# Performance work log

Hardware: AMD Instinct MI355X
Metric: run time of the kernel (lower is better)

## Reference

```python
import jax, jax.numpy as jnp
import numpy as np

B, T, C = 32, 2048, 1024  # batch, seq_len (<= block_size), n_embd
HEAD_SIZE = 128


def setup_inputs() -> dict:
    key = jax.random.key(0)
    kx, kk, kq, kv = jax.random.split(key, 4)
    std = 0.02  # CustomLinear init: normal(0, 0.02)
    return {
        "x": jax.random.normal(kx, (B, T, C), dtype=jnp.float32),
        "Wk": jax.random.normal(kk, (HEAD_SIZE, C), dtype=jnp.float32) * std,
        "Wq": jax.random.normal(kq, (HEAD_SIZE, C), dtype=jnp.float32) * std,
        "Wv": jax.random.normal(kv, (HEAD_SIZE, C), dtype=jnp.float32) * std,
    }


def reference(x, Wk, Wq, Wv):
    # x: [B, T, C]; W*: [head_size, C] (torch Linear layout, no bias)
    Bb, Tt, Cc = x.shape
    k = jnp.einsum("btc,hc->bth", x, Wk)
    q = jnp.einsum("btc,hc->bth", x, Wq)
    v = jnp.einsum("btc,hc->bth", x, Wv)
    # NOTE: original scales by C**-0.5 (n_embd), not head_size**-0.5
    wei = jnp.einsum("bth,bsh->bts", q, k) * (Cc ** -0.5)
    causal = jnp.tril(jnp.ones((Tt, Tt), dtype=bool))  # tril[:T,:T]
    wei = jnp.where(causal, wei, -jnp.inf)
    wei = jax.nn.softmax(wei, axis=-1)
    return jnp.einsum("bts,bsh->bth", wei, v)  # [B, T, head_size]
```

## Files before the change

### kernel.cpp

```cpp
#include <hip/hip_runtime.h>
#include <hip/hip_bf16.h>

typedef __bf16 bf8_t __attribute__((ext_vector_type(8)));
typedef __bf16 bf4_t __attribute__((ext_vector_type(4)));
typedef float f4_t __attribute__((ext_vector_type(4)));

#define B_ 32
#define T_ 2048
#define C_ 1024
#define H_ 128

__global__ __launch_bounds__(256) void wconv_kernel(
    const float* __restrict__ Wk, const float* __restrict__ Wq, const float* __restrict__ Wv,
    __bf16* __restrict__ Wb)
{
    const int e = (blockIdx.x * 256 + threadIdx.x) * 8;
    const int arr = e >> 17;
    const int off = e & 131071;
    const float* W = (arr == 0) ? Wk : (arr == 1) ? Wq : Wv;
    float4 f0 = *(const float4*)(W + off);
    float4 f1 = *(const float4*)(W + off + 4);
    bf8_t o;
    o[0] = (__bf16)f0.x; o[1] = (__bf16)f0.y; o[2] = (__bf16)f0.z; o[3] = (__bf16)f0.w;
    o[4] = (__bf16)f1.x; o[5] = (__bf16)f1.y; o[6] = (__bf16)f1.z; o[7] = (__bf16)f1.w;
    *(bf8_t*)(Wb + e) = o;
}

__global__ __launch_bounds__(256, 3) void proj_kernel(
    const float* __restrict__ x, const __bf16* __restrict__ Wb,
    __bf16* __restrict__ Kb, __bf16* __restrict__ Qb, __bf16* __restrict__ VtG)
{
    __shared__ __bf16 Xs[64][40];
    __shared__ __bf16 Ws[384][40];

    const int m0   = blockIdx.x * 64;
    const int tid  = threadIdx.x;
    const int lane = tid & 63;
    const int wn   = tid >> 6;
    const int lr   = lane & 15;
    const int quad = lane >> 4;

    f4_t acc[4][6];
    #pragma unroll
    for (int mi = 0; mi < 4; mi++)
        for (int ni = 0; ni < 6; ni++) acc[mi][ni] = f4_t{0.f, 0.f, 0.f, 0.f};

    float4 xr[2];
    bf8_t  wr[6];
    #pragma unroll
    for (int i = 0; i < 2; i++) {
        const int u = tid + i * 256;
        xr[i] = *(const float4*)(x + (size_t)(m0 + (u >> 3)) * C_ + ((u & 7) << 2));
    }
    #pragma unroll
    for (int i = 0; i < 6; i++) {
        const int u = tid + i * 256;
        wr[i] = *(const bf8_t*)(Wb + (size_t)(u >> 2) * C_ + ((u & 3) << 3));
    }

    for (int kkI = 0; kkI < 32; kkI++) {
        __syncthreads();
        #pragma unroll
        for (int i = 0; i < 2; i++) {
            const int u = tid + i * 256;
            float4 f = xr[i];
            *(bf4_t*)&Xs[u >> 3][(u & 7) << 2] =
                bf4_t{(__bf16)f.x, (__bf16)f.y, (__bf16)f.z, (__bf16)f.w};
        }
        #pragma unroll
        for (int i = 0; i < 6; i++) {
            const int u = tid + i * 256;
            *(bf8_t*)&Ws[u >> 2][(u & 3) << 3] = wr[i];
        }
        __syncthreads();
        if (kkI < 31) {
            const int kk = (kkI + 1) * 32;
            #pragma unroll
            for (int i = 0; i < 2; i++) {
                const int u = tid + i * 256;
                xr[i] = *(const float4*)(x + (size_t)(m0 + (u >> 3)) * C_ + kk + ((u & 7) << 2));
            }
            #pragma unroll
            for (int i = 0; i < 6; i++) {
                const int u = tid + i * 256;
                wr[i] = *(const bf8_t*)(Wb + (size_t)(u >> 2) * C_ + kk + ((u & 3) << 3));
            }
        }
        bf8_t xa[4];
        #pragma unroll
        for (int mi = 0; mi < 4; mi++) xa[mi] = *(const bf8_t*)&Xs[mi * 16 + lr][quad * 8];
        #pragma unroll
        for (int ni = 0; ni < 6; ni++) {
            bf8_t wb = *(const bf8_t*)&Ws[ni * 64 + wn * 16 + lr][quad * 8];
            if (ni < 4) {
                #pragma unroll
                for (int mi = 0; mi < 4; mi++)
                    acc[mi][ni] = __builtin_amdgcn_mfma_f32_16x16x32_bf16(xa[mi], wb, acc[mi][ni], 0, 0, 0);
            } else {
                #pragma unroll
                for (int mi = 0; mi < 4; mi++)
                    acc[mi][ni] = __builtin_amdgcn_mfma_f32_16x16x32_bf16(wb, xa[mi], acc[mi][ni], 0, 0, 0);
            }
        }
    }

    const int bb = m0 >> 11;
    const int t0 = m0 & (T_ - 1);
    #pragma unroll
    for (int ni = 0; ni < 4; ni++) {
        __bf16* Out = (ni < 2) ? Kb : Qb;
        const int col = (ni & 1) * 64 + wn * 16 + lr;
        #pragma unroll
        for (int mi = 0; mi < 4; mi++)
            for (int r = 0; r < 4; r++) {
                const int row = m0 + mi * 16 + quad * 4 + r;
                Out[(size_t)row * H_ + col] = (__bf16)acc[mi][ni][r];
            }
    }
    #pragma unroll
    for (int ni = 4; ni < 6; ni++)
        for (int mi = 0; mi < 4; mi++) {
            const int tok = t0 + mi * 16 + lr;
            #pragma unroll
            for (int r = 0; r < 4; r++) {
                const int h = (ni - 4) * 64 + wn * 16 + quad * 4 + r;
                VtG[(size_t)bb * H_ * T_ + (size_t)h * T_ + tok] = (__bf16)acc[mi][ni][r];
            }
        }
}

__global__ __launch_bounds__(512, 4) void flash_kernel(
    const __bf16* __restrict__ Qb, const __bf16* __restrict__ Kb,
    const __bf16* __restrict__ VtG, float* __restrict__ Out)
{
    __shared__ __bf16 Ks[64][136];
    __shared__ __bf16 Vt[128][72];
    __shared__ __bf16 Ps[128][72];

    const int qt = (blockIdx.y < 16) ? (15 - blockIdx.x) : blockIdx.x;
    const int b  = blockIdx.y;
    const size_t kqbase = (size_t)b * T_ * H_;
    const size_t vbase  = (size_t)b * H_ * T_;

    const int tid  = threadIdx.x;
    const int lane = tid & 63;
    const int w    = tid >> 6;
    const int lr   = lane & 15;
    const int quad = lane >> 4;

    bf8_t qf[4];
    {
        const __bf16* qp = Qb + kqbase + (size_t)(qt * 128 + w * 16 + lr) * H_ + quad * 8;
        #pragma unroll
        for (int ks = 0; ks < 4; ks++) qf[ks] = *(const bf8_t*)(qp + ks * 32);
    }

    f4_t o[8];
    #pragma unroll
    for (int n = 0; n < 8; n++) o[n] = f4_t{0.f, 0.f, 0.f, 0.f};
    float ls[4] = {0.f, 0.f, 0.f, 0.f};

    const float sc = 0.03125f * 1.4426950408889634f;
    const int jmax = 2 * qt + 1;

    const int kRow0 = tid >> 4,          kC0 = (tid & 15) << 3;
    const int kRow1 = (tid + 512) >> 4,  kC1 = ((tid + 512) & 15) << 3;
    const int vH0 = tid >> 3,            vS0 = (tid & 7) << 3;
    const int vH1 = (tid + 512) >> 3,    vS1 = ((tid + 512) & 7) << 3;

    bf8_t kr0 = *(const bf8_t*)(Kb + kqbase + (size_t)kRow0 * H_ + kC0);
    bf8_t kr1 = *(const bf8_t*)(Kb + kqbase + (size_t)kRow1 * H_ + kC1);
    bf8_t vr0 = *(const bf8_t*)(VtG + vbase + (size_t)vH0 * T_ + vS0);
    bf8_t vr1 = *(const bf8_t*)(VtG + vbase + (size_t)vH1 * T_ + vS1);

    for (int j = 0; j <= jmax; j++) {
        __syncthreads();
        *(bf8_t*)&Ks[kRow0][kC0] = kr0;
        *(bf8_t*)&Ks[kRow1][kC1] = kr1;
        *(bf8_t*)&Vt[vH0][vS0]   = vr0;
        *(bf8_t*)&Vt[vH1][vS1]   = vr1;
        __syncthreads();
        if (j < jmax) {
            const int s0 = (j + 1) * 64;
            kr0 = *(const bf8_t*)(Kb + kqbase + (size_t)(s0 + kRow0) * H_ + kC0);
            kr1 = *(const bf8_t*)(Kb + kqbase + (size_t)(s0 + kRow1) * H_ + kC1);
            vr0 = *(const bf8_t*)(VtG + vbase + (size_t)vH0 * T_ + s0 + vS0);
            vr1 = *(const bf8_t*)(VtG + vbase + (size_t)vH1 * T_ + s0 + vS1);
        }
        if (j == jmax && w < 4) continue;

        f4_t s4[4];
        #pragma unroll
        for (int n = 0; n < 4; n++) s4[n] = f4_t{0.f, 0.f, 0.f, 0.f};
        #pragma unroll
        for (int ks = 0; ks < 4; ks++)
            for (int n = 0; n < 4; n++) {
                bf8_t kf = *(const bf8_t*)&Ks[n * 16 + lr][ks * 32 + quad * 8];
                s4[n] = __builtin_amdgcn_mfma_f32_16x16x32_bf16(qf[ks], kf, s4[n], 0, 0, 0);
            }

        const bool domask = (j - 2 * qt) == (w >> 2);
        const int rowg = qt * 128 + w * 16 + quad * 4;
        #pragma unroll
        for (int n = 0; n < 4; n++) {
            const int colg = j * 64 + n * 16 + lr;
            #pragma unroll
            for (int r = 0; r < 4; r++) {
                float p = __builtin_exp2f(s4[n][r] * sc);
                if (domask && colg > rowg + r) p = 0.f;
                ls[r] += p;
                Ps[w * 16 + quad * 4 + r][n * 16 + lr] = (__bf16)p;
            }
        }

        #pragma unroll
        for (int ks = 0; ks < 2; ks++) {
            bf8_t pf = *(const bf8_t*)&Ps[w * 16 + lr][ks * 32 + quad * 8];
            #pragma unroll
            for (int n = 0; n < 8; n++) {
                bf8_t vf = *(const bf8_t*)&Vt[n * 16 + lr][ks * 32 + quad * 8];
                o[n] = __builtin_amdgcn_mfma_f32_16x16x32_bf16(pf, vf, o[n], 0, 0, 0);
            }
        }
    }

    float inv[4];
    #pragma unroll
    for (int r = 0; r < 4; r++) {
        float v = ls[r];
        v += __shfl_xor(v, 1);
        v += __shfl_xor(v, 2);
        v += __shfl_xor(v, 4);
        v += __shfl_xor(v, 8);
        inv[r] = 1.f / v;
    }
    #pragma unroll
    for (int n = 0; n < 8; n++) {
        const int col = n * 16 + lr;
        #pragma unroll
        for (int r = 0; r < 4; r++) {
            const int row = qt * 128 + w * 16 + quad * 4 + r;
            Out[kqbase + (size_t)row * H_ + col] = o[n][r] * inv[r];
        }
    }
}

extern "C" void kernel_launch(void* const* d_in, const int* in_sizes, int n_in,
                              void* d_out, int out_size, void* d_ws, size_t ws_size,
                              hipStream_t stream) {
    const float* x  = (const float*)d_in[0];
    const float* Wk = (const float*)d_in[1];
    const float* Wq = (const float*)d_in[2];
    const float* Wv = (const float*)d_in[3];
    float* out = (float*)d_out;

    const size_t n_kqv = (size_t)B_ * T_ * H_;
    __bf16* Kb  = (__bf16*)d_ws;
    __bf16* Qb  = Kb + n_kqv;
    __bf16* VtG = Qb + n_kqv;
    __bf16* Wb  = VtG + n_kqv;

    wconv_kernel<<<dim3(192), 256, 0, stream>>>(Wk, Wq, Wv, Wb);
    proj_kernel<<<dim3((B_ * T_) / 64), 256, 0, stream>>>(x, Wb, Kb, Qb, VtG);
    flash_kernel<<<dim3(16, B_), 512, 0, stream>>>(Qb, Kb, VtG, out);
}
```

Baseline: 512.1 us.

## Stage full x row tile in LDS and read pre-swizzled weights from global

The weight conversion kernel now writes bf16 weights in an MFMA-fragment-ordered layout, so the projection kernel can load weight operands directly from global/L2 instead of staging them through shared memory. The projection kernel keeps the whole 64x1024 x tile in LDS, loaded in 128-column chunks with register double-buffering, so there are fewer barriers per K step. The cost is much larger LDS use (about 129 KB), which drops occupancy to one block per CU (launch bounds changed to 1), and weight reads now depend on cache hits.

New measurement: 518.5 us. Within noise of the previous version (+1.3%).

```diff
diff --git a/kernel.cpp b/kernel.cpp
--- a/kernel.cpp
+++ b/kernel.cpp
@@ -12,26 +12,30 @@
 
 __global__ __launch_bounds__(256) void wconv_kernel(
     const float* __restrict__ Wk, const float* __restrict__ Wq, const float* __restrict__ Wv,
-    __bf16* __restrict__ Wb)
+    __bf16* __restrict__ Wr)
 {
-    const int e = (blockIdx.x * 256 + threadIdx.x) * 8;
-    const int arr = e >> 17;
-    const int off = e & 131071;
-    const float* W = (arr == 0) ? Wk : (arr == 1) ? Wq : Wv;
-    float4 f0 = *(const float4*)(W + off);
-    float4 f1 = *(const float4*)(W + off + 4);
+    const int e  = (blockIdx.x * 256 + threadIdx.x) * 8;
+    const int kk = e & 31;
+    const int lr = (e >> 5) & 15;
+    const int ks = (e >> 9) & 31;
+    const int cg = e >> 14;
+    const int col = cg * 16 + lr;
+    const int k   = ks * 32 + kk;
+    const float* W = (col < 128) ? Wk : (col < 256) ? Wq : Wv;
+    const float* p = W + (size_t)(col & 127) * C_ + k;
+    float4 f0 = *(const float4*)p;
+    float4 f1 = *(const float4*)(p + 4);
     bf8_t o;
     o[0] = (__bf16)f0.x; o[1] = (__bf16)f0.y; o[2] = (__bf16)f0.z; o[3] = (__bf16)f0.w;
     o[4] = (__bf16)f1.x; o[5] = (__bf16)f1.y; o[6] = (__bf16)f1.z; o[7] = (__bf16)f1.w;
-    *(bf8_t*)(Wb + e) = o;
-}
-
-__global__ __launch_bounds__(256, 3) void proj_kernel(
-    const float* __restrict__ x, const __bf16* __restrict__ Wb,
+    *(bf8_t*)(Wr + e) = o;
+}
+
+__global__ __launch_bounds__(256, 1) void proj_kernel(
+    const float* __restrict__ x, const __bf16* __restrict__ Wr,
     __bf16* __restrict__ Kb, __bf16* __restrict__ Qb, __bf16* __restrict__ VtG)
 {
-    __shared__ __bf16 Xs[64][40];
-    __shared__ __bf16 Ws[384][40];
+    __shared__ __bf16 Xs[64][C_ + 8];
 
     const int m0   = blockIdx.x * 64;
     const int tid  = threadIdx.x;
@@ -39,70 +43,69 @@
     const int wn   = tid >> 6;
     const int lr   = lane & 15;
     const int quad = lane >> 4;
+    const int r0   = tid >> 4;
+    const int kc   = (tid & 15) << 3;
 
     f4_t acc[4][6];
     #pragma unroll
     for (int mi = 0; mi < 4; mi++)
+        #pragma unroll
         for (int ni = 0; ni < 6; ni++) acc[mi][ni] = f4_t{0.f, 0.f, 0.f, 0.f};
 
-    float4 xr[2];
-    bf8_t  wr[6];
-    #pragma unroll
-    for (int i = 0; i < 2; i++) {
-        const int u = tid + i * 256;
-        xr[i] = *(const float4*)(x + (size_t)(m0 + (u >> 3)) * C_ + ((u & 7) << 2));
-    }
-    #pragma unroll
-    for (int i = 0; i < 6; i++) {
-        const int u = tid + i * 256;
-        wr[i] = *(const bf8_t*)(Wb + (size_t)(u >> 2) * C_ + ((u & 3) << 3));
-    }
-
-    for (int kkI = 0; kkI < 32; kkI++) {
-        __syncthreads();
-        #pragma unroll
-        for (int i = 0; i < 2; i++) {
-            const int u = tid + i * 256;
-            float4 f = xr[i];
-            *(bf4_t*)&Xs[u >> 3][(u & 7) << 2] =
-                bf4_t{(__bf16)f.x, (__bf16)f.y, (__bf16)f.z, (__bf16)f.w};
-        }
-        #pragma unroll
-        for (int i = 0; i < 6; i++) {
-            const int u = tid + i * 256;
-            *(bf8_t*)&Ws[u >> 2][(u & 3) << 3] = wr[i];
-        }
-        __syncthreads();
-        if (kkI < 31) {
-            const int kk = (kkI + 1) * 32;
-            #pragma unroll
-            for (int i = 0; i < 2; i++) {
-                const int u = tid + i * 256;
-                xr[i] = *(const float4*)(x + (size_t)(m0 + (u >> 3)) * C_ + kk + ((u & 7) << 2));
-            }
-            #pragma unroll
-            for (int i = 0; i < 6; i++) {
-                const int u = tid + i * 256;
-                wr[i] = *(const bf8_t*)(Wb + (size_t)(u >> 2) * C_ + kk + ((u & 3) << 3));
-            }
-        }
-        bf8_t xa[4];
-        #pragma unroll
-        for (int mi = 0; mi < 4; mi++) xa[mi] = *(const bf8_t*)&Xs[mi * 16 + lr][quad * 8];
-        #pragma unroll
-        for (int ni = 0; ni < 6; ni++) {
-            bf8_t wb = *(const bf8_t*)&Ws[ni * 64 + wn * 16 + lr][quad * 8];
-            if (ni < 4) {
-                #pragma unroll
-                for (int mi = 0; mi < 4; mi++)
-                    acc[mi][ni] = __builtin_amdgcn_mfma_f32_16x16x32_bf16(xa[mi], wb, acc[mi][ni], 0, 0, 0);
-            } else {
-                #pragma unroll
-                for (int mi = 0; mi < 4; mi++)
-                    acc[mi][ni] = __builtin_amdgcn_mfma_f32_16x16x32_bf16(wb, xa[mi], acc[mi][ni], 0, 0, 0);
-            }
-        }
-    }
+    float4 bufA[8], bufB[8];
+
+#define LOADC(buf, c) { _Pragma("unroll") \
+    for (int i_ = 0; i_ < 4; ++i_) { \
+        const float* p_ = x + (size_t)(m0 + r0 + i_ * 16) * C_ + (c) * 128 + kc; \
+        buf[2 * i_]     = *(const float4*)p_; \
+        buf[2 * i_ + 1] = *(const float4*)(p_ + 4); } }
+
+#define WRITEC(buf, c) { _Pragma("unroll") \
+    for (int i_ = 0; i_ < 4; ++i_) { \
+        float4 a_ = buf[2 * i_], b_ = buf[2 * i_ + 1]; \
+        bf8_t o_; \
+        o_[0] = (__bf16)a_.x; o_[1] = (__bf16)a_.y; o_[2] = (__bf16)a_.z; o_[3] = (__bf16)a_.w; \
+        o_[4] = (__bf16)b_.x; o_[5] = (__bf16)b_.y; o_[6] = (__bf16)b_.z; o_[7] = (__bf16)b_.w; \
+        *(bf8_t*)&Xs[r0 + i_ * 16][(c) * 128 + kc] = o_; } }
+
+#define COMPUTE(c) { _Pragma("unroll") \
+    for (int k4_ = 0; k4_ < 4; ++k4_) { \
+        const int ks_ = (c) * 4 + k4_; \
+        bf8_t xa_[4]; \
+        _Pragma("unroll") \
+        for (int mi = 0; mi < 4; ++mi) \
+            xa_[mi] = *(const bf8_t*)&Xs[mi * 16 + lr][ks_ * 32 + quad * 8]; \
+        _Pragma("unroll") \
+        for (int ni = 0; ni < 6; ++ni) { \
+            bf8_t wb_ = *(const bf8_t*)(Wr + (size_t)((ni * 4 + wn) * 32 + ks_) * 512 + lr * 32 + quad * 8); \
+            if (ni < 4) { \
+                _Pragma("unroll") \
+                for (int mi = 0; mi < 4; ++mi) \
+                    acc[mi][ni] = __builtin_amdgcn_mfma_f32_16x16x32_bf16(xa_[mi], wb_, acc[mi][ni], 0, 0, 0); \
+            } else { \
+                _Pragma("unroll") \
+                for (int mi = 0; mi < 4; ++mi) \
+                    acc[mi][ni] = __builtin_amdgcn_mfma_f32_16x16x32_bf16(wb_, xa_[mi], acc[mi][ni], 0, 0, 0); \
+            } } } }
+
+    LOADC(bufA, 0)
+    LOADC(bufB, 1)
+    WRITEC(bufA, 0)
+    __syncthreads();
+
+    #pragma unroll
+    for (int c = 0; c < 8; ++c) {
+        if (c < 6) { if (c & 1) LOADC(bufB, c + 2) else LOADC(bufA, c + 2) }
+        COMPUTE(c)
+        if (c < 7) {
+            if (c & 1) WRITEC(bufA, c + 1) else WRITEC(bufB, c + 1)
+            __syncthreads();
+        }
+    }
+
+#undef LOADC
+#undef WRITEC
+#undef COMPUTE
 
     const int bb = m0 >> 11;
     const int t0 = m0 & (T_ - 1);
@@ -258,9 +261,9 @@
     __bf16* Kb  = (__bf16*)d_ws;
     __bf16* Qb  = Kb + n_kqv;
     __bf16* VtG = Qb + n_kqv;
-    __bf16* Wb  = VtG + n_kqv;
-
-    wconv_kernel<<<dim3(192), 256, 0, stream>>>(Wk, Wq, Wv, Wb);
-    proj_kernel<<<dim3((B_ * T_) / 64), 256, 0, stream>>>(x, Wb, Kb, Qb, VtG);
+    __bf16* Wr  = VtG + n_kqv;
+
+    wconv_kernel<<<dim3(192), 256, 0, stream>>>(Wk, Wq, Wv, Wr);
+    proj_kernel<<<dim3((B_ * T_) / 64), 256, 0, stream>>>(x, Wr, Kb, Qb, VtG);
     flash_kernel<<<dim3(16, B_), 512, 0, stream>>>(Qb, Kb, VtG, out);
 }
```
